# Optimization experiments

Hardware: AMD Instinct MI355X
Metric: run time of the kernel (lower is better)

## Reference

```python
import jax, jax.numpy as jnp
import numpy as np

N, E, NFEAT, HID, HEADS, NCLASS = 100000, 1600000, 256, 64, 1, 32


def gat_conv(x, src, dst, W, a_src, a_dst, b, H, C, concat):
    n = x.shape[0]
    h = (x @ W).reshape(n, H, C)                      # [N,H,C]
    a_s = (h * a_src).sum(-1)                          # [N,H]
    a_d = (h * a_dst).sum(-1)                          # [N,H]
    e = jax.nn.leaky_relu(a_s[src] + a_d[dst], 0.2)    # [E,H]
    emax = jax.ops.segment_max(e, dst, num_segments=n)
    emax = jnp.where(jnp.isfinite(emax), emax, 0.0)
    ex = jnp.exp(e - emax[dst])
    denom = jax.ops.segment_sum(ex, dst, num_segments=n)
    alpha = ex / (denom[dst] + 1e-16)                  # segment softmax over in-edges of dst
    msg = h[src] * alpha[:, :, None]                   # [E,H,C]
    out = jax.ops.segment_sum(msg, dst, num_segments=n)
    out = out.reshape(n, H * C) if concat else out.mean(axis=1)
    return out + b


def setup_inputs() -> dict:
    key = jax.random.key(0)
    ks = jax.random.split(key, 14)
    x = jax.random.normal(ks[0], (N, NFEAT), dtype=jnp.float32)
    edge_index = jax.random.randint(ks[1], (2, E), 0, N, dtype=jnp.int64)
    s = 0.05
    return {
        'x': x, 'edge_index': edge_index,
        'W1': jax.random.normal(ks[2], (NFEAT, HEADS * HID), jnp.float32) * s,
        'as1': jax.random.normal(ks[3], (HEADS, HID), jnp.float32) * s,
        'ad1': jax.random.normal(ks[4], (HEADS, HID), jnp.float32) * s,
        'b1': jnp.zeros((HEADS * HID,), jnp.float32),
        'W2': jax.random.normal(ks[5], (HEADS * HID, HEADS * HID), jnp.float32) * s,
        'as2': jax.random.normal(ks[6], (HEADS, HID), jnp.float32) * s,
        'ad2': jax.random.normal(ks[7], (HEADS, HID), jnp.float32) * s,
        'b2': jnp.zeros((HEADS * HID,), jnp.float32),
        'W3': jax.random.normal(ks[8], (HEADS * HID, HEADS * NCLASS), jnp.float32) * s,
        'as3': jax.random.normal(ks[9], (HEADS, NCLASS), jnp.float32) * s,
        'ad3': jax.random.normal(ks[10], (HEADS, NCLASS), jnp.float32) * s,
        'b3': jnp.zeros((NCLASS,), jnp.float32),
    }


def reference(x, edge_index, W1, as1, ad1, b1, W2, as2, ad2, b2, W3, as3, ad3, b3):
    # add self loops (PyG GATConv add_self_loops=True)
    loop = jnp.arange(N, dtype=edge_index.dtype)
    src = jnp.concatenate([edge_index[0], loop])
    dst = jnp.concatenate([edge_index[1], loop])
    out = jax.nn.leaky_relu(gat_conv(x, src, dst, W1, as1, ad1, b1, HEADS, HID, True), 0.01)
    out = jax.nn.leaky_relu(gat_conv(out, src, dst, W2, as2, ad2, b2, HEADS, HID, True), 0.01)
    out = gat_conv(out, src, dst, W3, as3, ad3, b3, HEADS, NCLASS, False)
    return out
```

## Files before the change

kernel.cpp:

```cpp
#include <hip/hip_runtime.h>

#define NN 100000
#define NE 1600000
#define NF 256
#define HD 64
#define NC 32

#define BKS 8
#define NBK ((NN + 255) >> 8)
#define CHUNK 4096
#define NBLK ((NE + CHUNK - 1) / CHUNK)

__device__ __forceinline__ float lrelu02(float x) { return fmaxf(x, 0.2f * x); }

typedef __attribute__((ext_vector_type(8))) short bf16x8;
typedef __attribute__((ext_vector_type(4))) float f32x4;

__device__ __forceinline__ unsigned short f2bf(float f) {
    unsigned int u = __float_as_uint(f);
    unsigned int r = u + 0x7FFFu + ((u >> 16) & 1u);
    return (unsigned short)(r >> 16);
}
__device__ __forceinline__ float bf2f(unsigned short s) {
    return __uint_as_float(((unsigned int)s) << 16);
}


__global__ __launch_bounds__(256) void bucket_hist(const int* __restrict__ dst, int* __restrict__ gcnt) {
    __shared__ int hist[NBK];
    int tid = threadIdx.x;
    for (int i = tid; i < NBK; i += 256) hist[i] = 0;
    __syncthreads();
    int base = blockIdx.x * CHUNK;
    #pragma unroll
    for (int k = 0; k < CHUNK / 256; k++) {
        int i = base + k * 256 + tid;
        if (i < NE) atomicAdd(&hist[dst[i] >> BKS], 1);
    }
    __syncthreads();
    for (int i = tid; i < NBK; i += 256) if (hist[i]) atomicAdd(&gcnt[i], hist[i]);
}

__global__ void bucket_scan(const int* __restrict__ gcnt, int* __restrict__ gbase, int* __restrict__ gcur) {
    __shared__ int sh[512];
    int tid = threadIdx.x;
    int v = (tid < NBK) ? gcnt[tid] : 0;
    sh[tid] = v;
    __syncthreads();
    for (int d = 1; d < 512; d <<= 1) {
        int t = (tid >= d) ? sh[tid - d] : 0;
        __syncthreads();
        sh[tid] += t;
        __syncthreads();
    }
    if (tid < NBK) { int ex = sh[tid] - v; gbase[tid] = ex; gcur[tid] = ex; }
}

__global__ __launch_bounds__(256) void bin_edges(const int* __restrict__ src, const int* __restrict__ dst,
                                                 int* __restrict__ gcur, int2* __restrict__ ebuf) {
    __shared__ int hist[NBK];
    __shared__ int excl[NBK];
    __shared__ int runbase[NBK];
    __shared__ int ssum[256];
    __shared__ int2 sorted[CHUNK];
    int tid = threadIdx.x;
    int base = blockIdx.x * CHUNK;
    int n = NE - base; if (n > CHUNK) n = CHUNK;

    for (int i = tid; i < NBK; i += 256) hist[i] = 0;
    __syncthreads();

    int2 ed[CHUNK / 256];
    int bk[CHUNK / 256];
    #pragma unroll
    for (int k = 0; k < CHUNK / 256; k++) {
        int i = base + k * 256 + tid;
        if (i < NE) {
            ed[k] = make_int2(src[i], dst[i]);
            bk[k] = ed[k].y >> BKS;
            atomicAdd(&hist[bk[k]], 1);
        } else bk[k] = -1;
    }
    __syncthreads();
    int h0 = (2 * tid < NBK) ? hist[2 * tid] : 0;
    int h1 = (2 * tid + 1 < NBK) ? hist[2 * tid + 1] : 0;
    ssum[tid] = h0 + h1;
    __syncthreads();
    for (int d = 1; d < 256; d <<= 1) {
        int t = (tid >= d) ? ssum[tid - d] : 0;
        __syncthreads();
        ssum[tid] += t;
        __syncthreads();
    }
    int pref = ssum[tid] - (h0 + h1);
    if (2 * tid < NBK) excl[2 * tid] = pref;
    if (2 * tid + 1 < NBK) excl[2 * tid + 1] = pref + h0;
    for (int b = tid; b < NBK; b += 256) {
        int c = hist[b];
        runbase[b] = c ? atomicAdd(&gcur[b], c) : 0;
    }
    __syncthreads();
    #pragma unroll
    for (int k = 0; k < CHUNK / 256; k++) {
        if (bk[k] >= 0) {
            int r = atomicAdd(&excl[bk[k]], 1);
            sorted[r] = ed[k];
        }
    }
    __syncthreads();
    for (int i = tid; i < n; i += 256) {
        int2 e = sorted[i];
        int b = e.y >> BKS;
        int local_rank = i - (excl[b] - hist[b]);
        ebuf[runbase[b] + local_rank] = e;
    }
}

__global__ __launch_bounds__(256) void bucket_csr(const int2* __restrict__ ebuf, const int* __restrict__ gbase,
                                                  const int* __restrict__ gcnt,
                                                  int* __restrict__ offs, int* __restrict__ csr) {
    __shared__ int hist[256], cur[256], ssum[256];
    int b = blockIdx.x, tid = threadIdx.x;
    int ebeg = gbase[b], cnt = gcnt[b];
    int node0 = b << BKS;
    hist[tid] = 0;
    __syncthreads();
    for (int i = ebeg + tid; i < ebeg + cnt; i += 256)
        atomicAdd(&hist[ebuf[i].y & 255], 1);
    __syncthreads();
    int v = hist[tid];
    ssum[tid] = v;
    __syncthreads();
    for (int d = 1; d < 256; d <<= 1) {
        int t = (tid >= d) ? ssum[tid - d] : 0;
        __syncthreads();
        ssum[tid] += t;
        __syncthreads();
    }
    int ex = ebeg + ssum[tid] - v;
    cur[tid] = ex;
    int nnode = NN - node0; if (nnode > 256) nnode = 256;
    if (tid < nnode) offs[node0 + tid] = ex;
    if (b == NBK - 1 && tid == nnode - 1) offs[NN] = ebeg + cnt;
    __syncthreads();
    for (int i = ebeg + tid; i < ebeg + cnt; i += 256) {
        int2 e = ebuf[i];
        int pos = atomicAdd(&cur[e.y & 255], 1);
        csr[pos] = e.x;
    }
}


template <int CIN, int COUT>
__global__ __launch_bounds__(256) void mfma_gemm(const float* __restrict__ in, const float* __restrict__ W,
                                                 const float* __restrict__ a_s, const float* __restrict__ a_d,
                                                 float* __restrict__ h, float* __restrict__ asv,
                                                 float* __restrict__ adv) {
    const int KC  = 32;
    const int BM  = 128;
    const int RS  = 40;
    const int NCT = COUT / 16;
    const int NCH = CIN / KC;
    __shared__ unsigned short Ah[BM * RS];
    __shared__ unsigned short Al[BM * RS];
    __shared__ unsigned short Bh[COUT * RS];
    __shared__ unsigned short Bl[COUT * RS];

    int tid = threadIdx.x;
    int lane = tid & 63;
    int wave = tid >> 6;
    int fr = lane & 15;
    int kg = lane >> 4;
    int n0base = blockIdx.x * BM;

    f32x4 acc[2][NCT];
    #pragma unroll
    for (int rt = 0; rt < 2; rt++)
        #pragma unroll
        for (int ct = 0; ct < NCT; ct++) acc[rt][ct] = (f32x4){0.f, 0.f, 0.f, 0.f};

    for (int t = 0; t < NCH; t++) {
        int k0 = t * KC;
        __syncthreads();
        unsigned int* Ahu = (unsigned int*)Ah;
        unsigned int* Alu = (unsigned int*)Al;
        #pragma unroll
        for (int f = tid; f < BM * KC / 4; f += 256) {
            int row = f >> 3;
            int q = f & 7;
            int gn = n0base + row;
            float4 v = make_float4(0.f, 0.f, 0.f, 0.f);
            if (gn < NN) v = *(const float4*)&in[(size_t)gn * CIN + k0 + q * 4];
            unsigned short h0 = f2bf(v.x), h1 = f2bf(v.y), h2 = f2bf(v.z), h3 = f2bf(v.w);
            unsigned short l0 = f2bf(v.x - bf2f(h0)), l1 = f2bf(v.y - bf2f(h1));
            unsigned short l2 = f2bf(v.z - bf2f(h2)), l3 = f2bf(v.w - bf2f(h3));
            int wi = row * (RS / 2) + q * 2;
            Ahu[wi]     = (unsigned int)h0 | ((unsigned int)h1 << 16);
            Ahu[wi + 1] = (unsigned int)h2 | ((unsigned int)h3 << 16);
            Alu[wi]     = (unsigned int)l0 | ((unsigned int)l1 << 16);
            Alu[wi + 1] = (unsigned int)l2 | ((unsigned int)l3 << 16);
        }
        #pragma unroll
        for (int f = tid; f < KC * COUT / 4; f += 256) {
            int k = f / (COUT / 4);
            int c = (f % (COUT / 4)) * 4;
            float4 v = *(const float4*)&W[(size_t)(k0 + k) * COUT + c];
            unsigned short h0 = f2bf(v.x), h1 = f2bf(v.y), h2 = f2bf(v.z), h3 = f2bf(v.w);
            Bh[(c + 0) * RS + k] = h0;  Bl[(c + 0) * RS + k] = f2bf(v.x - bf2f(h0));
            Bh[(c + 1) * RS + k] = h1;  Bl[(c + 1) * RS + k] = f2bf(v.y - bf2f(h1));
            Bh[(c + 2) * RS + k] = h2;  Bl[(c + 2) * RS + k] = f2bf(v.z - bf2f(h2));
            Bh[(c + 3) * RS + k] = h3;  Bl[(c + 3) * RS + k] = f2bf(v.w - bf2f(h3));
        }
        __syncthreads();
        bf16x8 ah[2], al[2], bh[NCT], bl[NCT];
        #pragma unroll
        for (int rt = 0; rt < 2; rt++) {
            int row = wave * 32 + rt * 16 + fr;
            ah[rt] = *(const bf16x8*)&Ah[row * RS + kg * 8];
            al[rt] = *(const bf16x8*)&Al[row * RS + kg * 8];
        }
        #pragma unroll
        for (int ct = 0; ct < NCT; ct++) {
            int col = ct * 16 + fr;
            bh[ct] = *(const bf16x8*)&Bh[col * RS + kg * 8];
            bl[ct] = *(const bf16x8*)&Bl[col * RS + kg * 8];
        }
        #pragma unroll
        for (int rt = 0; rt < 2; rt++)
            #pragma unroll
            for (int ct = 0; ct < NCT; ct++) {
                acc[rt][ct] = __builtin_amdgcn_mfma_f32_16x16x32_bf16(ah[rt], bh[ct], acc[rt][ct], 0, 0, 0);
                acc[rt][ct] = __builtin_amdgcn_mfma_f32_16x16x32_bf16(ah[rt], bl[ct], acc[rt][ct], 0, 0, 0);
                acc[rt][ct] = __builtin_amdgcn_mfma_f32_16x16x32_bf16(al[rt], bh[ct], acc[rt][ct], 0, 0, 0);
            }
    }

    float As_l[NCT], Ad_l[NCT];
    #pragma unroll
    for (int ct = 0; ct < NCT; ct++) {
        As_l[ct] = a_s[ct * 16 + fr];
        Ad_l[ct] = a_d[ct * 16 + fr];
    }
    #pragma unroll
    for (int rt = 0; rt < 2; rt++) {
        #pragma unroll
        for (int r = 0; r < 4; r++) {
            int row = n0base + wave * 32 + rt * 16 + kg * 4 + r;
            if (row < NN) {
                #pragma unroll
                for (int ct = 0; ct < NCT; ct++)
                    h[(size_t)row * COUT + ct * 16 + fr] = acc[rt][ct][r];
            }
            float ps = 0.f, pd = 0.f;
            #pragma unroll
            for (int ct = 0; ct < NCT; ct++) {
                ps += acc[rt][ct][r] * As_l[ct];
                pd += acc[rt][ct][r] * Ad_l[ct];
            }
            #pragma unroll
            for (int off = 1; off < 16; off <<= 1) {
                ps += __shfl_xor(ps, off);
                pd += __shfl_xor(pd, off);
            }
            if (fr == 0 && row < NN) { asv[row] = ps; adv[row] = pd; }
        }
    }
}


template <int C, bool ACT>
__global__ __launch_bounds__(256) void gat_agg(const float* __restrict__ h, const float* __restrict__ asv,
                                               const float* __restrict__ adv, const int* __restrict__ offs,
                                               const int* __restrict__ csr,
                                               const float* __restrict__ bias, float* __restrict__ out) {
    const int LPR = C / 4;
    const int G = 64 / LPR;
    const float4* h4 = (const float4*)h;
    int lane = threadIdx.x & 63;
    int v = blockIdx.x * 4 + (threadIdx.x >> 6);
    int beg = offs[v], end = offs[v + 1];
    int g = lane / LPR, r = lane % LPR;
    float adv_v = adv[v];

    float4 acc = {0.f, 0.f, 0.f, 0.f};
    float dsum = 0.f;
    #pragma unroll 4
    for (int e = beg + g; e < end; e += G) {
        int s = csr[e];
        float ww = __expf(lrelu02(asv[s] + adv_v));
        float4 hv = h4[(size_t)s * LPR + r];
        dsum += ww;
        acc.x += ww * hv.x; acc.y += ww * hv.y; acc.z += ww * hv.z; acc.w += ww * hv.w;
    }
    #pragma unroll
    for (int off = LPR; off < 64; off <<= 1) {
        acc.x += __shfl_xor(acc.x, off);
        acc.y += __shfl_xor(acc.y, off);
        acc.z += __shfl_xor(acc.z, off);
        acc.w += __shfl_xor(acc.w, off);
        dsum += __shfl_xor(dsum, off);
    }
    if (g == 0) {
        float selfw = __expf(lrelu02(asv[v] + adv_v));
        float4 hs = h4[(size_t)v * LPR + r];
        acc.x += selfw * hs.x; acc.y += selfw * hs.y;
        acc.z += selfw * hs.z; acc.w += selfw * hs.w;
        dsum += selfw;
        float inv = 1.f / (dsum + 1e-16f);
        float4 bb = ((const float4*)bias)[r];
        float4 o;
        o.x = acc.x * inv + bb.x; o.y = acc.y * inv + bb.y;
        o.z = acc.z * inv + bb.z; o.w = acc.w * inv + bb.w;
        if (ACT) {
            o.x = fmaxf(o.x, 0.01f * o.x); o.y = fmaxf(o.y, 0.01f * o.y);
            o.z = fmaxf(o.z, 0.01f * o.z); o.w = fmaxf(o.w, 0.01f * o.w);
        }
        ((float4*)out)[(size_t)v * LPR + r] = o;
    }
}


extern "C" void kernel_launch(void* const* d_in, const int* in_sizes, int n_in,
                              void* d_out, int out_size, void* d_ws, size_t ws_size,
                              hipStream_t stream) {
    const float* x   = (const float*)d_in[0];
    const int*   ei  = (const int*)d_in[1];
    const float* W1  = (const float*)d_in[2];
    const float* as1 = (const float*)d_in[3];
    const float* ad1 = (const float*)d_in[4];
    const float* b1  = (const float*)d_in[5];
    const float* W2  = (const float*)d_in[6];
    const float* as2 = (const float*)d_in[7];
    const float* ad2 = (const float*)d_in[8];
    const float* b2  = (const float*)d_in[9];
    const float* W3  = (const float*)d_in[10];
    const float* as3 = (const float*)d_in[11];
    const float* ad3 = (const float*)d_in[12];
    const float* b3  = (const float*)d_in[13];
    float* out = (float*)d_out;

    const int* srcp = ei;
    const int* dstp = ei + NE;

    char* w = (char*)d_ws;
    float* h     = (float*)w;   w += sizeof(float) * (size_t)NN * HD;
    float* featB = (float*)w;   w += sizeof(float) * (size_t)NN * HD;
    float* asv   = (float*)w;   w += sizeof(float) * NN;
    float* advv  = (float*)w;   w += sizeof(float) * NN;
    int* offs    = (int*)w;     w += sizeof(int) * (NN + 1);
    int* csr     = (int*)w;     w += sizeof(int) * (size_t)NE;
    int2* ebuf   = (int2*)w;    w += sizeof(int2) * (size_t)NE;
    int* gcnt    = (int*)w;     w += sizeof(int) * NBK;
    int* gbase   = (int*)w;     w += sizeof(int) * NBK;
    int* gcur    = (int*)w;     w += sizeof(int) * NBK;

    const int GBM = (NN + 127) / 128;

    hipMemsetAsync(gcnt, 0, sizeof(int) * NBK, stream);
    bucket_hist<<<NBLK, 256, 0, stream>>>(dstp, gcnt);
    bucket_scan<<<1, 512, 0, stream>>>(gcnt, gbase, gcur);
    bin_edges<<<NBLK, 256, 0, stream>>>(srcp, dstp, gcur, ebuf);
    bucket_csr<<<NBK, 256, 0, stream>>>(ebuf, gbase, gcnt, offs, csr);

    mfma_gemm<NF, HD><<<GBM, 256, 0, stream>>>(x, W1, as1, ad1, h, asv, advv);
    gat_agg<HD, true><<<NN / 4, 256, 0, stream>>>(h, asv, advv, offs, csr, b1, featB);

    mfma_gemm<HD, HD><<<GBM, 256, 0, stream>>>(featB, W2, as2, ad2, h, asv, advv);
    gat_agg<HD, true><<<NN / 4, 256, 0, stream>>>(h, asv, advv, offs, csr, b2, featB);

    mfma_gemm<HD, NC><<<GBM, 256, 0, stream>>>(featB, W3, as3, ad3, h, asv, advv);
    gat_agg<NC, false><<<NN / 4, 256, 0, stream>>>(h, asv, advv, offs, csr, b3, out);
}
```

Measured before the change: 461.2 us.

## Double-buffer GEMM LDS tiles with register prefetch and k-group-major layout

Restructures the split-bf16 MFMA GEMM so the next K chunk of inputs and weights is loaded into registers while MFMAs run on the current LDS buffer, then written to the alternate buffer. This drops one barrier per iteration. The LDS layout becomes k-group-major ([kgroup][row][8]), and each thread now loads a column of W and writes packed vectors instead of scalar transposed stores, which cuts bank conflicts and store count. The cost is double the LDS footprint and more live registers, which may lower occupancy.

```diff
diff --git a/kernel.cpp b/kernel.cpp
--- a/kernel.cpp
+++ b/kernel.cpp
@@ -23,6 +23,15 @@
 }
 __device__ __forceinline__ float bf2f(unsigned short s) {
     return __uint_as_float(((unsigned int)s) << 16);
+}
+__device__ __forceinline__ void split4(float4 v, uint2& hi, uint2& lo) {
+    unsigned short h0 = f2bf(v.x), h1 = f2bf(v.y), h2 = f2bf(v.z), h3 = f2bf(v.w);
+    unsigned short l0 = f2bf(v.x - bf2f(h0)), l1 = f2bf(v.y - bf2f(h1));
+    unsigned short l2 = f2bf(v.z - bf2f(h2)), l3 = f2bf(v.w - bf2f(h3));
+    hi.x = (unsigned int)h0 | ((unsigned int)h1 << 16);
+    hi.y = (unsigned int)h2 | ((unsigned int)h3 << 16);
+    lo.x = (unsigned int)l0 | ((unsigned int)l1 << 16);
+    lo.y = (unsigned int)l2 | ((unsigned int)l3 << 16);
 }
 
 
@@ -158,81 +167,118 @@
                                                  float* __restrict__ adv) {
     const int KC  = 32;
     const int BM  = 128;
-    const int RS  = 40;
     const int NCT = COUT / 16;
     const int NCH = CIN / KC;
-    __shared__ unsigned short Ah[BM * RS];
-    __shared__ unsigned short Al[BM * RS];
-    __shared__ unsigned short Bh[COUT * RS];
-    __shared__ unsigned short Bl[COUT * RS];
-
-    int tid = threadIdx.x;
+    const int TPC = 256 / COUT;
+    const int KPER = KC / TPC;
+
+    __shared__ unsigned short Ah[2][4 * BM * 8];
+    __shared__ unsigned short Al[2][4 * BM * 8];
+    __shared__ unsigned short Bh[2][4 * COUT * 8];
+    __shared__ unsigned short Bl[2][4 * COUT * 8];
+
+    int tid  = threadIdx.x;
     int lane = tid & 63;
     int wave = tid >> 6;
     int fr = lane & 15;
     int kg = lane >> 4;
     int n0base = blockIdx.x * BM;
 
+    int wcol = tid % COUT;
+    int kseg = tid / COUT;
+    int kb   = kseg * KPER;
+    int kgW  = kb >> 3;
+    int kofW = kb & 7;
+
+    float4 xr[4];
+    float  wreg[KPER];
+
     f32x4 acc[2][NCT];
     #pragma unroll
     for (int rt = 0; rt < 2; rt++)
         #pragma unroll
         for (int ct = 0; ct < NCT; ct++) acc[rt][ct] = (f32x4){0.f, 0.f, 0.f, 0.f};
 
-    for (int t = 0; t < NCH; t++) {
-        int k0 = t * KC;
-        __syncthreads();
-        unsigned int* Ahu = (unsigned int*)Ah;
-        unsigned int* Alu = (unsigned int*)Al;
-        #pragma unroll
-        for (int f = tid; f < BM * KC / 4; f += 256) {
-            int row = f >> 3;
-            int q = f & 7;
+    auto load_regs = [&](int k0) {
+        #pragma unroll
+        for (int i = 0; i < 4; i++) {
+            int f = tid + i * 256;
+            int row = f >> 3, q = f & 7;
             int gn = n0base + row;
-            float4 v = make_float4(0.f, 0.f, 0.f, 0.f);
-            if (gn < NN) v = *(const float4*)&in[(size_t)gn * CIN + k0 + q * 4];
-            unsigned short h0 = f2bf(v.x), h1 = f2bf(v.y), h2 = f2bf(v.z), h3 = f2bf(v.w);
-            unsigned short l0 = f2bf(v.x - bf2f(h0)), l1 = f2bf(v.y - bf2f(h1));
-            unsigned short l2 = f2bf(v.z - bf2f(h2)), l3 = f2bf(v.w - bf2f(h3));
-            int wi = row * (RS / 2) + q * 2;
-            Ahu[wi]     = (unsigned int)h0 | ((unsigned int)h1 << 16);
-            Ahu[wi + 1] = (unsigned int)h2 | ((unsigned int)h3 << 16);
-            Alu[wi]     = (unsigned int)l0 | ((unsigned int)l1 << 16);
-            Alu[wi + 1] = (unsigned int)l2 | ((unsigned int)l3 << 16);
-        }
-        #pragma unroll
-        for (int f = tid; f < KC * COUT / 4; f += 256) {
-            int k = f / (COUT / 4);
-            int c = (f % (COUT / 4)) * 4;
-            float4 v = *(const float4*)&W[(size_t)(k0 + k) * COUT + c];
-            unsigned short h0 = f2bf(v.x), h1 = f2bf(v.y), h2 = f2bf(v.z), h3 = f2bf(v.w);
-            Bh[(c + 0) * RS + k] = h0;  Bl[(c + 0) * RS + k] = f2bf(v.x - bf2f(h0));
-            Bh[(c + 1) * RS + k] = h1;  Bl[(c + 1) * RS + k] = f2bf(v.y - bf2f(h1));
-            Bh[(c + 2) * RS + k] = h2;  Bl[(c + 2) * RS + k] = f2bf(v.z - bf2f(h2));
-            Bh[(c + 3) * RS + k] = h3;  Bl[(c + 3) * RS + k] = f2bf(v.w - bf2f(h3));
-        }
-        __syncthreads();
-        bf16x8 ah[2], al[2], bh[NCT], bl[NCT];
+            xr[i] = make_float4(0.f, 0.f, 0.f, 0.f);
+            if (gn < NN) xr[i] = *(const float4*)&in[(size_t)gn * CIN + k0 + q * 4];
+        }
+        #pragma unroll
+        for (int j = 0; j < KPER; j++)
+            wreg[j] = W[(size_t)(k0 + kb + j) * COUT + wcol];
+    };
+
+    auto write_lds = [&](int buf) {
+        #pragma unroll
+        for (int i = 0; i < 4; i++) {
+            int f = tid + i * 256;
+            int row = f >> 3, q = f & 7;
+            int akg = q >> 1, off = (q & 1) * 4;
+            uint2 hi, lo;
+            split4(xr[i], hi, lo);
+            *(uint2*)&Ah[buf][(akg * BM + row) * 8 + off] = hi;
+            *(uint2*)&Al[buf][(akg * BM + row) * 8 + off] = lo;
+        }
+        unsigned short bh8[8], bl8[8];
+        #pragma unroll
+        for (int j = 0; j < KPER; j++) {
+            bh8[j] = f2bf(wreg[j]);
+            bl8[j] = f2bf(wreg[j] - bf2f(bh8[j]));
+        }
+        if constexpr (KPER == 8) {
+            uint4 ph = make_uint4((unsigned)bh8[0] | ((unsigned)bh8[1] << 16), (unsigned)bh8[2] | ((unsigned)bh8[3] << 16),
+                                  (unsigned)bh8[4] | ((unsigned)bh8[5] << 16), (unsigned)bh8[6] | ((unsigned)bh8[7] << 16));
+            uint4 pl = make_uint4((unsigned)bl8[0] | ((unsigned)bl8[1] << 16), (unsigned)bl8[2] | ((unsigned)bl8[3] << 16),
+                                  (unsigned)bl8[4] | ((unsigned)bl8[5] << 16), (unsigned)bl8[6] | ((unsigned)bl8[7] << 16));
+            *(uint4*)&Bh[buf][(kgW * COUT + wcol) * 8 + kofW] = ph;
+            *(uint4*)&Bl[buf][(kgW * COUT + wcol) * 8 + kofW] = pl;
+        } else {
+            uint2 ph = make_uint2((unsigned)bh8[0] | ((unsigned)bh8[1] << 16), (unsigned)bh8[2] | ((unsigned)bh8[3] << 16));
+            uint2 pl = make_uint2((unsigned)bl8[0] | ((unsigned)bl8[1] << 16), (unsigned)bl8[2] | ((unsigned)bl8[3] << 16));
+            *(uint2*)&Bh[buf][(kgW * COUT + wcol) * 8 + kofW] = ph;
+            *(uint2*)&Bl[buf][(kgW * COUT + wcol) * 8 + kofW] = pl;
+        }
+    };
+
+    auto do_mfma = [&](int buf) {
+        bf16x8 ah[2], al[2];
         #pragma unroll
         for (int rt = 0; rt < 2; rt++) {
             int row = wave * 32 + rt * 16 + fr;
-            ah[rt] = *(const bf16x8*)&Ah[row * RS + kg * 8];
-            al[rt] = *(const bf16x8*)&Al[row * RS + kg * 8];
+            ah[rt] = *(const bf16x8*)&Ah[buf][(kg * BM + row) * 8];
+            al[rt] = *(const bf16x8*)&Al[buf][(kg * BM + row) * 8];
         }
         #pragma unroll
         for (int ct = 0; ct < NCT; ct++) {
             int col = ct * 16 + fr;
-            bh[ct] = *(const bf16x8*)&Bh[col * RS + kg * 8];
-            bl[ct] = *(const bf16x8*)&Bl[col * RS + kg * 8];
-        }
-        #pragma unroll
-        for (int rt = 0; rt < 2; rt++)
+            bf16x8 bh = *(const bf16x8*)&Bh[buf][(kg * COUT + col) * 8];
+            bf16x8 bl = *(const bf16x8*)&Bl[buf][(kg * COUT + col) * 8];
             #pragma unroll
-            for (int ct = 0; ct < NCT; ct++) {
-                acc[rt][ct] = __builtin_amdgcn_mfma_f32_16x16x32_bf16(ah[rt], bh[ct], acc[rt][ct], 0, 0, 0);
-                acc[rt][ct] = __builtin_amdgcn_mfma_f32_16x16x32_bf16(ah[rt], bl[ct], acc[rt][ct], 0, 0, 0);
-                acc[rt][ct] = __builtin_amdgcn_mfma_f32_16x16x32_bf16(al[rt], bh[ct], acc[rt][ct], 0, 0, 0);
+            for (int rt = 0; rt < 2; rt++) {
+                acc[rt][ct] = __builtin_amdgcn_mfma_f32_16x16x32_bf16(ah[rt], bh, acc[rt][ct], 0, 0, 0);
+                acc[rt][ct] = __builtin_amdgcn_mfma_f32_16x16x32_bf16(ah[rt], bl, acc[rt][ct], 0, 0, 0);
+                acc[rt][ct] = __builtin_amdgcn_mfma_f32_16x16x32_bf16(al[rt], bh, acc[rt][ct], 0, 0, 0);
             }
+        }
+    };
+
+    load_regs(0);
+    write_lds(0);
+    __syncthreads();
+
+    for (int t = 0; t < NCH; t++) {
+        int cur = t & 1;
+        if (t + 1 < NCH) load_regs((t + 1) * KC);
+        do_mfma(cur);
+        if (t + 1 < NCH) {
+            write_lds(cur ^ 1);
+            __syncthreads();
+        }
     }
 
     float As_l[NCT], Ad_l[NCT];
```

New measurement: 454.5 us. About the same (-1.4%).
